# Kernel tuning notes

Hardware: AMD Instinct MI355X
Metric: run time of the kernel (lower is better)

## Reference

```python
import jax, jax.numpy as jnp
import numpy as np

STRIDE = (1, 1)
PADDING = ((1, 1), (1, 1))


def setup_inputs() -> dict:
    key = jax.random.key(0)
    k1, k2 = jax.random.split(key)
    x = jax.random.normal(k1, (32, 256, 56, 56), dtype=jnp.float32)
    # kaiming-uniform-like init scale (matches _ConvNd.reset_parameters magnitude roughly)
    fan_in = 256 * 3 * 3
    bound = float(np.sqrt(1.0 / fan_in))
    weight = jax.random.uniform(k2, (256, 256, 3, 3), dtype=jnp.float32,
                                minval=-bound, maxval=bound)
    return {"x": x, "weight": weight}


def reference(x, weight):
    # per-output-filter mean of |w| over (in_ch, kh, kw)
    a = jnp.mean(jnp.abs(weight), axis=(1, 2, 3), keepdims=True)  # [O,1,1,1]
    b = jnp.sign(weight)
    binary_weight = b * a
    out = jax.lax.conv_general_dilated(
        x, binary_weight,
        window_strides=STRIDE,
        padding=PADDING,
        dimension_numbers=("NCHW", "OIHW", "NCHW"),
    )
    return out
```

## Files before the change

kernel.cpp:

```cpp
#include <hip/hip_runtime.h>
#include <cstdint>
#include <cstddef>

#define XP_BYTES 55115776ull
#define WB_OFF   55115776ull
#define AL_OFF   (WB_OFF + 1179648ull)

typedef __bf16 bf16x8 __attribute__((ext_vector_type(8)));
typedef float  f32x4  __attribute__((ext_vector_type(4)));
typedef unsigned short u16x8 __attribute__((ext_vector_type(8)));

static __device__ __forceinline__ unsigned short f2bf(float f) {
  union { float f; unsigned int u; } v; v.f = f;
  unsigned int u = v.u;
  u += 0x7FFFu + ((u >> 16) & 1u);
  return (unsigned short)(u >> 16);
}

static __device__ __forceinline__ void async16(void* lds, const void* g) {
  __builtin_amdgcn_global_load_lds(
      (const __attribute__((address_space(1))) unsigned int*)g,
      (__attribute__((address_space(3))) unsigned int*)lds, 16, 0, 0);
}

__global__ void prep_w(const float* __restrict__ w, unsigned short* __restrict__ wb,
                       float* __restrict__ alpha) {
  const int o = blockIdx.x, c = threadIdx.x;
  const float* wr = w + (size_t)(o * 256 + c) * 9;
  float s = 0.f;
#pragma unroll
  for (int tap = 0; tap < 9; ++tap) {
    float v = wr[tap];
    s += fabsf(v);
    unsigned short sg = (v > 0.f) ? 0x3F80u : ((v < 0.f) ? 0xBF80u : 0u);
    wb[(size_t)o * 2304 + tap * 256 + c] = sg;
  }
  __shared__ float red[256];
  red[c] = s;
  __syncthreads();
  for (int d = 128; d > 0; d >>= 1) {
    if (c < d) red[c] += red[c + d];
    __syncthreads();
  }
  if (c == 0) alpha[o] = red[0] * (1.f / 2304.f);
}

__global__ void zero_halo(unsigned short* __restrict__ xp) {
  const int n = blockIdx.x;
  const int t = threadIdx.x;
  uint32_t* base = (uint32_t*)(xp + (size_t)n * 58 * 58 * 256);
  uint32_t* r57 = base + 57 * 7424;
  for (int i = t; i < 7424; i += 1024) { base[i] = 0; r57[i] = 0; }
  for (int i = t; i < 7168; i += 1024) {
    const int r = i >> 7, c = i & 127;
    base[(size_t)((r + 1) * 58) * 128 + c] = 0;
    base[(size_t)((r + 1) * 58 + 57) * 128 + c] = 0;
  }
}

__global__ void prep_x(const float* __restrict__ x, unsigned short* __restrict__ xp) {
  __shared__ unsigned short tile[64 * 256];
  const int bx = blockIdx.x;
  const int n = bx / 49, pt = bx % 49;
  const int p0 = pt * 64;
  const int tid = threadIdx.x;
  const int f = tid & 15;
  const int cg = tid >> 4;
  const float* xn = x + (size_t)n * 256 * 3136 + p0 + f * 4;

#pragma unroll
  for (int i = 0; i < 16; ++i) {
    const int c = cg + i * 16;
    const float4 v = *(const float4*)(xn + (size_t)c * 3136);
    unsigned short b[4] = {f2bf(v.x), f2bf(v.y), f2bf(v.z), f2bf(v.w)};
#pragma unroll
    for (int j = 0; j < 4; ++j) {
      const int pix = f * 4 + j;
      const int cs = c ^ (((pix >> 2) & 3) << 3) ^ (((pix >> 4) & 3) << 5);
      tile[pix * 256 + cs] = b[j];
    }
  }
  __syncthreads();

  const int c8 = (tid & 31) * 8;
  const int psub = tid >> 5;
#pragma unroll
  for (int pass = 0; pass < 8; ++pass) {
    const int pl = psub + pass * 8;
    const int p = p0 + pl;
    const int h = p / 56, w = p % 56;
    const int cs = c8 ^ (((pl >> 2) & 3) << 3) ^ (((pl >> 4) & 3) << 5);
    const u16x8 v = *(const u16x8*)&tile[pl * 256 + cs];
    *(u16x8*)(xp + ((size_t)(n * 58 + h + 1) * 58 + (w + 1)) * 256 + c8) = v;
  }
}

__global__ __launch_bounds__(256, 2)
void conv_mfma(const unsigned short* __restrict__ xp,
               const unsigned short* __restrict__ wb,
               const float* __restrict__ alpha,
               float* __restrict__ out) {
  __shared__ __align__(16) char lds[32768];

  const int tid = threadIdx.x;
  const int wave = tid >> 6, lane = tid & 63;
  const int wm = wave >> 1, wn = wave & 1;
  const int o0 = (blockIdx.x & 1) * 128;
  const int pix0 = (blockIdx.x >> 1) * 128;

  const int chunk = lane & 3;
  const int rsub = lane >> 2;

  const char* wbB = (const char*)wb;
  const char* xpB = (const char*)xp;
  const char* gA[2];
  const char* gB[2];
#pragma unroll
  for (int j = 0; j < 2; ++j) {
    const int row = (wave * 2 + j) * 16 + rsub;
    gA[j] = wbB + ((size_t)(o0 + row) * 2304 + chunk * 8) * 2;
    const int pix = pix0 + row;
    const int n = pix / 3136, rem = pix % 3136;
    const int h = rem / 56, w = rem % 56;
    gB[j] = xpB + (size_t)((n * 58 + h) * 58 + w) * 512 + chunk * 16;
  }

  f32x4 acc[4][4];
#pragma unroll
  for (int i = 0; i < 4; ++i)
#pragma unroll
    for (int j = 0; j < 4; ++j) acc[i][j] = (f32x4){0.f, 0.f, 0.f, 0.f};

  const int ar = lane & 15, aq = lane >> 4;

  auto stage = [&](int b, int ks) {
    const int tap = ks >> 3;
    const int tapoff = ((tap / 3) * 58 + (tap % 3)) * 512;
    const int kA = ks * 64;
    const int kB = tapoff + (ks & 7) * 64;
    char* LA = lds + b * 16384;
    char* LB = LA + 8192;
    async16(LA + (wave * 2 + 0) * 1024, gA[0] + kA);
    async16(LA + (wave * 2 + 1) * 1024, gA[1] + kA);
    async16(LB + (wave * 2 + 0) * 1024, gB[0] + kB);
    async16(LB + (wave * 2 + 1) * 1024, gB[1] + kB);
  };

  stage(0, 0);
#pragma unroll 2
  for (int ks = 0; ks < 72; ++ks) {
    const int cur = ks & 1;
    __syncthreads();
    if (ks < 71) stage(cur ^ 1, ks + 1);

    const char* LA = lds + cur * 16384;
    const char* LB = LA + 8192;
    bf16x8 af[4], bfr[4];
#pragma unroll
    for (int mi = 0; mi < 4; ++mi)
      af[mi] = *(const bf16x8*)(LA + ((wm * 64 + mi * 16 + ar) * 64 + aq * 16));
#pragma unroll
    for (int ni = 0; ni < 4; ++ni)
      bfr[ni] = *(const bf16x8*)(LB + ((wn * 64 + ni * 16 + ar) * 64 + aq * 16));
#pragma unroll
    for (int mi = 0; mi < 4; ++mi)
#pragma unroll
      for (int ni = 0; ni < 4; ++ni)
        acc[mi][ni] = __builtin_amdgcn_mfma_f32_16x16x32_bf16(af[mi], bfr[ni], acc[mi][ni], 0, 0, 0);
  }

  int nc[4], rc[4];
#pragma unroll
  for (int ni = 0; ni < 4; ++ni) {
    const int pix = pix0 + wn * 64 + ni * 16 + ar;
    nc[ni] = pix / 3136; rc[ni] = pix % 3136;
  }
#pragma unroll
  for (int mi = 0; mi < 4; ++mi) {
    const int orow = o0 + wm * 64 + mi * 16 + aq * 4;
    float al[4];
#pragma unroll
    for (int r = 0; r < 4; ++r) al[r] = alpha[orow + r];
#pragma unroll
    for (int ni = 0; ni < 4; ++ni) {
      const size_t base = (size_t)nc[ni] * 802816 + (size_t)orow * 3136 + (size_t)rc[ni];
#pragma unroll
      for (int r = 0; r < 4; ++r)
        out[base + (size_t)r * 3136] = acc[mi][ni][r] * al[r];
    }
  }
}

extern "C" void kernel_launch(void* const* d_in, const int* in_sizes, int n_in,
                              void* d_out, int out_size, void* d_ws, size_t ws_size,
                              hipStream_t stream) {
  const float* x = (const float*)d_in[0];
  const float* w = (const float*)d_in[1];
  char* ws = (char*)d_ws;
  unsigned short* xp  = (unsigned short*)ws;
  unsigned short* wbp = (unsigned short*)(ws + WB_OFF);
  float* alpha = (float*)(ws + AL_OFF);
  float* out = (float*)d_out;

  zero_halo<<<32, 1024, 0, stream>>>(xp);
  prep_w<<<256, 256, 0, stream>>>(w, wbp, alpha);
  prep_x<<<32 * 49, 256, 0, stream>>>(x, xp);
  conv_mfma<<<1568, 256, 0, stream>>>(xp, wbp, alpha, out);
}
```

Before: 346.8 us.

## Enlarge conv tile to all 256 outputs with triple-buffered LDS pipeline

Each block now computes all 256 output channels for a 128-pixel tile (an 8x4 MFMA accumulator grid per wave) instead of 128x128, so the grid halves and each input pixel tile is loaded once rather than twice. The K loop moves from a double buffer to a triple buffer with explicit vmcnt waits and raw barriers, and raises wave priority around the MFMA block. LDS reads use an XOR swizzle on the 16-byte chunks to avoid bank conflicts, and the block index is remapped to spread pixel tiles across the grid. In exchange the kernel uses more registers (128 accumulator floats) and 72KB of LDS per block, which limits occupancy.

```diff
diff --git a/kernel.cpp b/kernel.cpp
--- a/kernel.cpp
+++ b/kernel.cpp
@@ -100,74 +100,103 @@
                const unsigned short* __restrict__ wb,
                const float* __restrict__ alpha,
                float* __restrict__ out) {
-  __shared__ __align__(16) char lds[32768];
+  __shared__ __align__(16) char lds[73728];
 
   const int tid = threadIdx.x;
   const int wave = tid >> 6, lane = tid & 63;
-  const int wm = wave >> 1, wn = wave & 1;
-  const int o0 = (blockIdx.x & 1) * 128;
-  const int pix0 = (blockIdx.x >> 1) * 128;
-
-  const int chunk = lane & 3;
-  const int rsub = lane >> 2;
+  const int wm = wave & 1, wn = wave >> 1;
+
+  const int ptile = (blockIdx.x & 7) * 98 + (blockIdx.x >> 3);
+  const int pix0 = ptile * 128;
+
+  const int rsub  = lane >> 2;
+  const int chunk = (lane & 3) ^ ((rsub >> 1) & 3);
 
   const char* wbB = (const char*)wb;
   const char* xpB = (const char*)xp;
-  const char* gA[2];
+  const char* gA[4];
   const char* gB[2];
 #pragma unroll
+  for (int j = 0; j < 4; ++j) {
+    const int row = wave * 64 + j * 16 + rsub;
+    gA[j] = wbB + ((size_t)row * 2304 + chunk * 8) * 2;
+  }
+#pragma unroll
   for (int j = 0; j < 2; ++j) {
-    const int row = (wave * 2 + j) * 16 + rsub;
-    gA[j] = wbB + ((size_t)(o0 + row) * 2304 + chunk * 8) * 2;
-    const int pix = pix0 + row;
+    const int prow = wave * 32 + j * 16 + rsub;
+    const int pix = pix0 + prow;
     const int n = pix / 3136, rem = pix % 3136;
     const int h = rem / 56, w = rem % 56;
     gB[j] = xpB + (size_t)((n * 58 + h) * 58 + w) * 512 + chunk * 16;
   }
 
-  f32x4 acc[4][4];
-#pragma unroll
-  for (int i = 0; i < 4; ++i)
+  f32x4 acc[8][4];
+#pragma unroll
+  for (int i = 0; i < 8; ++i)
 #pragma unroll
     for (int j = 0; j < 4; ++j) acc[i][j] = (f32x4){0.f, 0.f, 0.f, 0.f};
 
   const int ar = lane & 15, aq = lane >> 4;
-
-  auto stage = [&](int b, int ks) {
+  const int axor = ((ar >> 1) & 3) * 16;
+
+  auto stage = [&](int buf, int ks) {
     const int tap = ks >> 3;
-    const int tapoff = ((tap / 3) * 58 + (tap % 3)) * 512;
+    const int kh = (tap * 11) >> 5;
+    const int kw = tap - kh * 3;
     const int kA = ks * 64;
-    const int kB = tapoff + (ks & 7) * 64;
-    char* LA = lds + b * 16384;
-    char* LB = LA + 8192;
-    async16(LA + (wave * 2 + 0) * 1024, gA[0] + kA);
-    async16(LA + (wave * 2 + 1) * 1024, gA[1] + kA);
-    async16(LB + (wave * 2 + 0) * 1024, gB[0] + kB);
-    async16(LB + (wave * 2 + 1) * 1024, gB[1] + kB);
+    const int kB = (kh * 58 + kw) * 512 + (ks & 7) * 64;
+    char* base = lds + buf * 24576;
+#pragma unroll
+    for (int j = 0; j < 4; ++j)
+      async16(base + (wave * 4 + j) * 1024, gA[j] + kA);
+#pragma unroll
+    for (int j = 0; j < 2; ++j)
+      async16(base + 16384 + (wave * 2 + j) * 1024, gB[j] + kB);
   };
 
-  stage(0, 0);
-#pragma unroll 2
-  for (int ks = 0; ks < 72; ++ks) {
-    const int cur = ks & 1;
-    __syncthreads();
-    if (ks < 71) stage(cur ^ 1, ks + 1);
-
-    const char* LA = lds + cur * 16384;
-    const char* LB = LA + 8192;
-    bf16x8 af[4], bfr[4];
-#pragma unroll
-    for (int mi = 0; mi < 4; ++mi)
-      af[mi] = *(const bf16x8*)(LA + ((wm * 64 + mi * 16 + ar) * 64 + aq * 16));
+  auto step = [&](int buf) {
+    const char* LA = lds + buf * 24576;
+    const char* LB = LA + 16384;
+    bf16x8 af[8], bfr[4];
+#pragma unroll
+    for (int mi = 0; mi < 8; ++mi)
+      af[mi] = *(const bf16x8*)(LA + ((wm * 128 + mi * 16 + ar) * 64 + (aq * 16 ^ axor)));
 #pragma unroll
     for (int ni = 0; ni < 4; ++ni)
-      bfr[ni] = *(const bf16x8*)(LB + ((wn * 64 + ni * 16 + ar) * 64 + aq * 16));
-#pragma unroll
-    for (int mi = 0; mi < 4; ++mi)
+      bfr[ni] = *(const bf16x8*)(LB + ((wn * 64 + ni * 16 + ar) * 64 + (aq * 16 ^ axor)));
+    __builtin_amdgcn_s_setprio(1);
+#pragma unroll
+    for (int mi = 0; mi < 8; ++mi)
 #pragma unroll
       for (int ni = 0; ni < 4; ++ni)
         acc[mi][ni] = __builtin_amdgcn_mfma_f32_16x16x32_bf16(af[mi], bfr[ni], acc[mi][ni], 0, 0, 0);
-  }
+    __builtin_amdgcn_s_setprio(0);
+  };
+
+#define ROUND(buf, t)                                   \
+  asm volatile("s_waitcnt vmcnt(6)" ::: "memory");      \
+  __builtin_amdgcn_s_barrier();                         \
+  asm volatile("" ::: "memory");                        \
+  stage(((buf) + 2) % 3, (t) + 2);                      \
+  step(buf);
+
+  stage(0, 0);
+  stage(1, 1);
+  for (int t3 = 0; t3 < 69; t3 += 3) {
+    ROUND(0, t3)
+    ROUND(1, t3 + 1)
+    ROUND(2, t3 + 2)
+  }
+  ROUND(0, 69)
+  asm volatile("s_waitcnt vmcnt(6)" ::: "memory");
+  __builtin_amdgcn_s_barrier();
+  asm volatile("" ::: "memory");
+  step(1);
+  asm volatile("s_waitcnt vmcnt(0)" ::: "memory");
+  __builtin_amdgcn_s_barrier();
+  asm volatile("" ::: "memory");
+  step(2);
+#undef ROUND
 
   int nc[4], rc[4];
 #pragma unroll
@@ -176,8 +205,8 @@
     nc[ni] = pix / 3136; rc[ni] = pix % 3136;
   }
 #pragma unroll
-  for (int mi = 0; mi < 4; ++mi) {
-    const int orow = o0 + wm * 64 + mi * 16 + aq * 4;
+  for (int mi = 0; mi < 8; ++mi) {
+    const int orow = wm * 128 + mi * 16 + aq * 4;
     float al[4];
 #pragma unroll
     for (int r = 0; r < 4; ++r) al[r] = alpha[orow + r];
@@ -205,5 +234,5 @@
   zero_halo<<<32, 1024, 0, stream>>>(xp);
   prep_w<<<256, 256, 0, stream>>>(w, wbp, alpha);
   prep_x<<<32 * 49, 256, 0, stream>>>(x, xp);
-  conv_mfma<<<1568, 256, 0, stream>>>(xp, wbp, alpha, out);
-}
+  conv_mfma<<<784, 256, 0, stream>>>(xp, wbp, alpha, out);
+}
```

New measurement: 312.7 us. 1.11x faster.

## Drop LDS staging; load MFMA fragments directly from global with register double-buffering

Applied to the files above, without the earlier changes.

The conv kernel no longer stages A/B tiles through LDS with async global-to-LDS copies and block barriers. Each wave now loads its bf16 fragments straight from global memory into registers, double-buffered across k-steps. Each block covers all 256 output channels for 128 pixels (8x4 fragments per wave), with a swizzled block-to-tile mapping, so the launch is halved. This removes barrier and LDS traffic but gives up cross-wave sharing of loads, leaning on L1/L2 instead, and raises register pressure (128 accumulator floats plus 24 fragment vectors per lane), which risks occupancy loss or spills.

```diff
diff --git a/kernel.cpp b/kernel.cpp
--- a/kernel.cpp
+++ b/kernel.cpp
@@ -15,12 +15,6 @@
   unsigned int u = v.u;
   u += 0x7FFFu + ((u >> 16) & 1u);
   return (unsigned short)(u >> 16);
-}
-
-static __device__ __forceinline__ void async16(void* lds, const void* g) {
-  __builtin_amdgcn_global_load_lds(
-      (const __attribute__((address_space(1))) unsigned int*)g,
-      (__attribute__((address_space(3))) unsigned int*)lds, 16, 0, 0);
 }
 
 __global__ void prep_w(const float* __restrict__ w, unsigned short* __restrict__ wb,
@@ -100,74 +94,76 @@
                const unsigned short* __restrict__ wb,
                const float* __restrict__ alpha,
                float* __restrict__ out) {
-  __shared__ __align__(16) char lds[32768];
-
   const int tid = threadIdx.x;
   const int wave = tid >> 6, lane = tid & 63;
-  const int wm = wave >> 1, wn = wave & 1;
-  const int o0 = (blockIdx.x & 1) * 128;
-  const int pix0 = (blockIdx.x >> 1) * 128;
-
-  const int chunk = lane & 3;
-  const int rsub = lane >> 2;
+  const int wm = wave & 1, wn = wave >> 1;
+
+  const int ptile = (blockIdx.x & 7) * 98 + (blockIdx.x >> 3);
+  const int pix0 = ptile * 128;
+
+  const int ar = lane & 15, aq = lane >> 4;
 
   const char* wbB = (const char*)wb;
   const char* xpB = (const char*)xp;
-  const char* gA[2];
-  const char* gB[2];
-#pragma unroll
-  for (int j = 0; j < 2; ++j) {
-    const int row = (wave * 2 + j) * 16 + rsub;
-    gA[j] = wbB + ((size_t)(o0 + row) * 2304 + chunk * 8) * 2;
-    const int pix = pix0 + row;
+
+  const char* aP[8];
+#pragma unroll
+  for (int mi = 0; mi < 8; ++mi)
+    aP[mi] = wbB + ((size_t)(wm * 128 + mi * 16 + ar) * 2304 + aq * 8) * 2;
+
+  const char* bP[4];
+#pragma unroll
+  for (int ni = 0; ni < 4; ++ni) {
+    const int pix = pix0 + wn * 64 + ni * 16 + ar;
     const int n = pix / 3136, rem = pix % 3136;
     const int h = rem / 56, w = rem % 56;
-    gB[j] = xpB + (size_t)((n * 58 + h) * 58 + w) * 512 + chunk * 16;
-  }
-
-  f32x4 acc[4][4];
-#pragma unroll
-  for (int i = 0; i < 4; ++i)
+    bP[ni] = xpB + (size_t)((n * 58 + h) * 58 + w) * 512 + aq * 16;
+  }
+
+  f32x4 acc[8][4];
+#pragma unroll
+  for (int i = 0; i < 8; ++i)
 #pragma unroll
     for (int j = 0; j < 4; ++j) acc[i][j] = (f32x4){0.f, 0.f, 0.f, 0.f};
 
-  const int ar = lane & 15, aq = lane >> 4;
-
-  auto stage = [&](int b, int ks) {
-    const int tap = ks >> 3;
-    const int tapoff = ((tap / 3) * 58 + (tap % 3)) * 512;
-    const int kA = ks * 64;
-    const int kB = tapoff + (ks & 7) * 64;
-    char* LA = lds + b * 16384;
-    char* LB = LA + 8192;
-    async16(LA + (wave * 2 + 0) * 1024, gA[0] + kA);
-    async16(LA + (wave * 2 + 1) * 1024, gA[1] + kA);
-    async16(LB + (wave * 2 + 0) * 1024, gB[0] + kB);
-    async16(LB + (wave * 2 + 1) * 1024, gB[1] + kB);
-  };
-
-  stage(0, 0);
-#pragma unroll 2
-  for (int ks = 0; ks < 72; ++ks) {
-    const int cur = ks & 1;
-    __syncthreads();
-    if (ks < 71) stage(cur ^ 1, ks + 1);
-
-    const char* LA = lds + cur * 16384;
-    const char* LB = LA + 8192;
-    bf16x8 af[4], bfr[4];
-#pragma unroll
-    for (int mi = 0; mi < 4; ++mi)
-      af[mi] = *(const bf16x8*)(LA + ((wm * 64 + mi * 16 + ar) * 64 + aq * 16));
-#pragma unroll
-    for (int ni = 0; ni < 4; ++ni)
-      bfr[ni] = *(const bf16x8*)(LB + ((wn * 64 + ni * 16 + ar) * 64 + aq * 16));
-#pragma unroll
-    for (int mi = 0; mi < 4; ++mi)
-#pragma unroll
-      for (int ni = 0; ni < 4; ++ni)
-        acc[mi][ni] = __builtin_amdgcn_mfma_f32_16x16x32_bf16(af[mi], bfr[ni], acc[mi][ni], 0, 0, 0);
-  }
+  bf16x8 afA[8], afB[8], bfA[4], bfB[4];
+
+#define LOADF(AF, BF, t)                                                     \
+  do {                                                                       \
+    const int _tap = (t) >> 3;                                               \
+    const int _kh = (_tap * 11) >> 5;                                        \
+    const int _ob = (_kh * 58 + (_tap - _kh * 3)) * 512 + ((t) & 7) * 64;    \
+    const int _oa = (t) * 64;                                                \
+    _Pragma("unroll")                                                        \
+    for (int mi = 0; mi < 8; ++mi)                                           \
+      AF[mi] = *(const bf16x8*)(aP[mi] + _oa);                               \
+    _Pragma("unroll")                                                        \
+    for (int ni = 0; ni < 4; ++ni)                                           \
+      BF[ni] = *(const bf16x8*)(bP[ni] + _ob);                               \
+  } while (0)
+
+#define MFMAS(AF, BF)                                                        \
+  do {                                                                       \
+    _Pragma("unroll")                                                        \
+    for (int mi = 0; mi < 8; ++mi)                                           \
+      _Pragma("unroll")                                                      \
+      for (int ni = 0; ni < 4; ++ni)                                         \
+        acc[mi][ni] = __builtin_amdgcn_mfma_f32_16x16x32_bf16(               \
+            AF[mi], BF[ni], acc[mi][ni], 0, 0, 0);                           \
+  } while (0)
+
+  LOADF(afA, bfA, 0);
+  for (int t = 0; t < 70; t += 2) {
+    LOADF(afB, bfB, t + 1);
+    MFMAS(afA, bfA);
+    LOADF(afA, bfA, t + 2);
+    MFMAS(afB, bfB);
+  }
+  LOADF(afB, bfB, 71);
+  MFMAS(afA, bfA);
+  MFMAS(afB, bfB);
+#undef LOADF
+#undef MFMAS
 
   int nc[4], rc[4];
 #pragma unroll
@@ -176,8 +172,8 @@
     nc[ni] = pix / 3136; rc[ni] = pix % 3136;
   }
 #pragma unroll
-  for (int mi = 0; mi < 4; ++mi) {
-    const int orow = o0 + wm * 64 + mi * 16 + aq * 4;
+  for (int mi = 0; mi < 8; ++mi) {
+    const int orow = wm * 128 + mi * 16 + aq * 4;
     float al[4];
 #pragma unroll
     for (int r = 0; r < 4; ++r) al[r] = alpha[orow + r];
@@ -205,5 +201,5 @@
   zero_halo<<<32, 1024, 0, stream>>>(xp);
   prep_w<<<256, 256, 0, stream>>>(w, wbp, alpha);
   prep_x<<<32 * 49, 256, 0, stream>>>(x, xp);
-  conv_mfma<<<1568, 256, 0, stream>>>(xp, wbp, alpha, out);
-}
+  conv_mfma<<<784, 256, 0, stream>>>(xp, wbp, alpha, out);
+}
```

Result: slower. 569.9 us (+64.4%).

## Rewrite conv GEMM as 256x256 tile, 8-wave ping-pong pipeline with swizzled LDS

Applied to the files above, without the earlier changes.

The conv GEMM kernel moves to 512-thread blocks computing a 256-output x 256-pixel tile with a 128KB double-buffered LDS and a K-step of 128 per stage. The loop is split into phased quadrants, with explicit barriers, waitcnt and setprio, so async global->LDS loads overlap the MFMA work. LDS rows are XOR-swizzled to cut bank conflicts, and the pixel-tile order is remapped across blocks. The aim is more data reuse per loaded byte and hidden load latency, at the cost of one block per CU and higher register pressure.

```diff
diff --git a/kernel.cpp b/kernel.cpp
--- a/kernel.cpp
+++ b/kernel.cpp
@@ -95,79 +95,150 @@
   }
 }
 
-__global__ __launch_bounds__(256, 2)
+__global__ __launch_bounds__(512, 1)
 void conv_mfma(const unsigned short* __restrict__ xp,
                const unsigned short* __restrict__ wb,
                const float* __restrict__ alpha,
                float* __restrict__ out) {
-  __shared__ __align__(16) char lds[32768];
+  __shared__ __align__(16) char lds[131072];
 
   const int tid = threadIdx.x;
   const int wave = tid >> 6, lane = tid & 63;
-  const int wm = wave >> 1, wn = wave & 1;
-  const int o0 = (blockIdx.x & 1) * 128;
-  const int pix0 = (blockIdx.x >> 1) * 128;
-
-  const int chunk = lane & 3;
+  const int wm = wave & 1, wn = wave >> 1;
+
+  const int ptile = (blockIdx.x & 7) * 49 + (blockIdx.x >> 3);
+  const int pix0 = ptile * 256;
+
+  const int ar = lane & 15, aq = lane >> 4;
+  const int rpos = (aq ^ ((ar >> 1) & 3)) * 16;
   const int rsub = lane >> 2;
+  const int chunkS = (lane & 3) ^ ((rsub >> 1) & 3);
 
   const char* wbB = (const char*)wb;
   const char* xpB = (const char*)xp;
-  const char* gA[2];
-  const char* gB[2];
+
+  const char* aSrc[2]; int aDst[2];
+  const char* bSrcP[2][2]; int bDst[2];
 #pragma unroll
   for (int j = 0; j < 2; ++j) {
-    const int row = (wave * 2 + j) * 16 + rsub;
-    gA[j] = wbB + ((size_t)(o0 + row) * 2304 + chunk * 8) * 2;
-    const int pix = pix0 + row;
-    const int n = pix / 3136, rem = pix % 3136;
-    const int h = rem / 56, w = rem % 56;
-    gB[j] = xpB + (size_t)((n * 58 + h) * 58 + w) * 512 + chunk * 16;
-  }
-
-  f32x4 acc[4][4];
-#pragma unroll
-  for (int i = 0; i < 4; ++i)
+    const int idx = j * 8 + wave;
+    const int ksS = idx & 1, grp = idx >> 1;
+    const int rowNP = (grp & 3) * 16 + ((grp >> 2) << 7);
+    aSrc[j] = wbB + (size_t)(rowNP + rsub) * 4608 + ksS * 64 + chunkS * 16;
+    aDst[j] = ksS * 16384 + rowNP * 64;
+    const int pixNP = (grp >> 1) * 64 + (grp & 1) * 16;
+#pragma unroll
+    for (int par = 0; par < 2; ++par) {
+      const int pix = pix0 + pixNP + par * 32 + rsub;
+      const int n = pix / 3136, rem = pix % 3136;
+      const int h = rem / 56, w = rem % 56;
+      bSrcP[par][j] = xpB + (size_t)((n * 58 + h) * 58 + w) * 512 + ksS * 64 + chunkS * 16;
+    }
+    bDst[j] = 65536 + ksS * 16384 + pixNP * 64;
+  }
+
+  f32x4 acc[8][4];
+#pragma unroll
+  for (int i = 0; i < 8; ++i)
 #pragma unroll
     for (int j = 0; j < 4; ++j) acc[i][j] = (f32x4){0.f, 0.f, 0.f, 0.f};
 
-  const int ar = lane & 15, aq = lane >> 4;
-
-  auto stage = [&](int b, int ks) {
-    const int tap = ks >> 3;
-    const int tapoff = ((tap / 3) * 58 + (tap % 3)) * 512;
-    const int kA = ks * 64;
-    const int kB = tapoff + (ks & 7) * 64;
-    char* LA = lds + b * 16384;
-    char* LB = LA + 8192;
-    async16(LA + (wave * 2 + 0) * 1024, gA[0] + kA);
-    async16(LA + (wave * 2 + 1) * 1024, gA[1] + kA);
-    async16(LB + (wave * 2 + 0) * 1024, gB[0] + kB);
-    async16(LB + (wave * 2 + 1) * 1024, gB[1] + kB);
-  };
-
-  stage(0, 0);
-#pragma unroll 2
-  for (int ks = 0; ks < 72; ++ks) {
-    const int cur = ks & 1;
-    __syncthreads();
-    if (ks < 71) stage(cur ^ 1, ks + 1);
-
-    const char* LA = lds + cur * 16384;
-    const char* LB = LA + 8192;
-    bf16x8 af[4], bfr[4];
-#pragma unroll
-    for (int mi = 0; mi < 4; ++mi)
-      af[mi] = *(const bf16x8*)(LA + ((wm * 64 + mi * 16 + ar) * 64 + aq * 16));
-#pragma unroll
-    for (int ni = 0; ni < 4; ++ni)
-      bfr[ni] = *(const bf16x8*)(LB + ((wn * 64 + ni * 16 + ar) * 64 + aq * 16));
-#pragma unroll
-    for (int mi = 0; mi < 4; ++mi)
-#pragma unroll
-      for (int ni = 0; ni < 4; ++ni)
-        acc[mi][ni] = __builtin_amdgcn_mfma_f32_16x16x32_bf16(af[mi], bfr[ni], acc[mi][ni], 0, 0, 0);
-  }
+  bf16x8 af[4][2], bfE[2][2], bfO[2][2];
+
+  auto stageA = [&](int b, int T, int par) {
+    const size_t so = (size_t)par * 294912 + (size_t)T * 128;
+    const int dof = par * 4096 + b * 32768;
+#pragma unroll
+    for (int j = 0; j < 2; ++j)
+      async16(lds + aDst[j] + dof, aSrc[j] + so);
+  };
+  auto stageB = [&](int b, int T, int par) {
+    const int tap = T >> 2;
+    const int kh = (tap * 11) >> 5, kw = tap - kh * 3;
+    const int ob = (kh * 58 + kw) * 512 + (T & 3) * 128;
+    const int dof = par * 2048 + b * 32768;
+#pragma unroll
+    for (int j = 0; j < 2; ++j)
+      async16(lds + bDst[j] + dof, bSrcP[par][j] + ob);
+  };
+  auto readA = [&](int b, int mh) {
+    const char* base = lds + b * 32768;
+#pragma unroll
+    for (int q = 0; q < 4; ++q)
+#pragma unroll
+      for (int ks = 0; ks < 2; ++ks)
+        af[q][ks] = *(const bf16x8*)(base + ks * 16384 +
+                      (wm * 128 + mh * 64 + q * 16 + ar) * 64 + rpos);
+  };
+  auto readB = [&](int b, int nh, bf16x8 (*bf)[2]) {
+    const char* base = lds + 65536 + b * 32768;
+#pragma unroll
+    for (int q = 0; q < 2; ++q)
+#pragma unroll
+      for (int ks = 0; ks < 2; ++ks)
+        bf[q][ks] = *(const bf16x8*)(base + ks * 16384 +
+                      (wn * 64 + nh * 32 + q * 16 + ar) * 64 + rpos);
+  };
+  auto mmaQ = [&](int mh, int nh, bf16x8 (*bf)[2]) {
+    __builtin_amdgcn_s_setprio(1);
+#pragma unroll
+    for (int ks = 0; ks < 2; ++ks)
+#pragma unroll
+      for (int q = 0; q < 4; ++q)
+#pragma unroll
+        for (int r = 0; r < 2; ++r)
+          acc[mh * 4 + q][nh * 2 + r] = __builtin_amdgcn_mfma_f32_16x16x32_bf16(
+              af[q][ks], bf[r][ks], acc[mh * 4 + q][nh * 2 + r], 0, 0, 0);
+    __builtin_amdgcn_s_setprio(0);
+  };
+
+#define PH_SYNC                                          \
+  asm volatile("" ::: "memory");                         \
+  __builtin_amdgcn_s_barrier();                          \
+  asm volatile("s_waitcnt lgkmcnt(0)" ::: "memory");     \
+  __builtin_amdgcn_sched_barrier(0);
+#define PH_END                                           \
+  asm volatile("" ::: "memory");                         \
+  __builtin_amdgcn_s_barrier();
+
+  stageA(0, 0, 0); stageB(0, 0, 1); stageA(0, 0, 1); stageB(0, 0, 0);
+  stageA(1, 1, 0); stageB(1, 1, 1);
+  asm volatile("s_waitcnt vmcnt(4)" ::: "memory");
+  PH_END;
+
+  for (int i = 0; i < 18; ++i) {
+    const int T0 = 2 * i, T1 = 2 * i + 1;
+    const bool pf = (i < 17);
+    readA(0, 0); readB(0, 0, bfE);
+    stageA(1, T1, 1);
+    PH_SYNC; mmaQ(0, 0, bfE); PH_END;
+    readB(0, 1, bfO);
+    stageB(1, T1, 0);
+    PH_SYNC; mmaQ(0, 1, bfO); PH_END;
+    readA(0, 1);
+    if (pf) stageA(0, T0 + 2, 0);
+    PH_SYNC; mmaQ(1, 1, bfO); PH_END;
+    if (pf) stageB(0, T0 + 2, 1);
+    PH_SYNC; mmaQ(1, 0, bfE);
+    if (pf) { asm volatile("s_waitcnt vmcnt(4)" ::: "memory"); }
+    else    { asm volatile("s_waitcnt vmcnt(0)" ::: "memory"); }
+    PH_END;
+    readA(1, 0); readB(1, 0, bfE);
+    if (pf) stageA(0, T0 + 2, 1);
+    PH_SYNC; mmaQ(0, 0, bfE); PH_END;
+    readB(1, 1, bfO);
+    if (pf) stageB(0, T0 + 2, 0);
+    PH_SYNC; mmaQ(0, 1, bfO); PH_END;
+    readA(1, 1);
+    if (pf) stageA(1, T1 + 2, 0);
+    PH_SYNC; mmaQ(1, 1, bfO); PH_END;
+    if (pf) stageB(1, T1 + 2, 1);
+    PH_SYNC; mmaQ(1, 0, bfE);
+    if (pf) { asm volatile("s_waitcnt vmcnt(4)" ::: "memory"); }
+    PH_END;
+  }
+#undef PH_SYNC
+#undef PH_END
 
   int nc[4], rc[4];
 #pragma unroll
@@ -176,8 +247,8 @@
     nc[ni] = pix / 3136; rc[ni] = pix % 3136;
   }
 #pragma unroll
-  for (int mi = 0; mi < 4; ++mi) {
-    const int orow = o0 + wm * 64 + mi * 16 + aq * 4;
+  for (int mi = 0; mi < 8; ++mi) {
+    const int orow = wm * 128 + mi * 16 + aq * 4;
     float al[4];
 #pragma unroll
     for (int r = 0; r < 4; ++r) al[r] = alpha[orow + r];
@@ -205,5 +276,5 @@
   zero_halo<<<32, 1024, 0, stream>>>(xp);
   prep_w<<<256, 256, 0, stream>>>(w, wbp, alpha);
   prep_x<<<32 * 49, 256, 0, stream>>>(x, xp);
-  conv_mfma<<<1568, 256, 0, stream>>>(xp, wbp, alpha, out);
-}
+  conv_mfma<<<392, 512, 0, stream>>>(xp, wbp, alpha, out);
+}
```

Measured after the change: 303.1 us. 1.14x faster.
